# Kernel optimization log

Measured on AMD Instinct MI355X. Metric: run time of the kernel, lower is better.

## Reference

```python
import jax, jax.numpy as jnp
import numpy as np

B, D, H1, H2, J, Q, O = 32768, 35, 256, 256, 12, 7, 5


def setup_inputs() -> dict:
    key = jax.random.key(0)
    ks = jax.random.split(key, 16)
    s = 0.05
    inp = {
        "x": jax.random.uniform(ks[0], (B, D), dtype=jnp.float32),
        "judge_ids": jax.random.randint(ks[1], (B,), 0, J, dtype=jnp.int32),
        # shared layers
        "W1_w": jax.random.normal(ks[2], (H1, D + 1), jnp.float32) * s,
        "W1_b": jnp.zeros((H1,), jnp.float32),
        "W2_w": jax.random.normal(ks[3], (H2, H1 + 1), jnp.float32) * s,
        "W2_b": jnp.zeros((H2,), jnp.float32),
        # judge-specific layers (stacked over J experts)
        "W1a_w": jax.random.normal(ks[4], (J, H1, D + 1), jnp.float32) * s,
        "W1a_b": jnp.zeros((J, H1), jnp.float32),
        "W2a_w": jax.random.normal(ks[5], (J, H2, H1 + 1), jnp.float32) * s,
        "W2a_b": jnp.zeros((J, H2), jnp.float32),
        # per-question output heads (shared + judge-specific)
        "V_w": jax.random.normal(ks[6], (Q, O, H2 + 1), jnp.float32) * s,
        "V_b": jnp.zeros((Q, O), jnp.float32),
        "Va_w": jax.random.normal(ks[7], (J, Q, O, H2 + 1), jnp.float32) * s,
        "Va_b": jnp.zeros((J, Q, O), jnp.float32),
    }
    return inp


def _append_ones(a):
    return jnp.concatenate([a, jnp.ones((a.shape[0], 1), a.dtype)], axis=1)


def reference(x, judge_ids, W1_w, W1_b, W2_w, W2_b, W1a_w, W1a_b, W2a_w, W2a_b, V_w, V_b, Va_w, Va_b):
    ids = judge_ids.astype(jnp.int32)
    xb = _append_ones(x)                                   # (B, D+1)
    # layer 1: shared + judge-routed
    a1 = jnp.einsum('bi,jhi->bjh', xb, W1a_w)              # (B, J, H1)
    j1 = jnp.take_along_axis(a1, ids[:, None, None], axis=1)[:, 0] + W1a_b[ids]
    z1 = jax.nn.relu(xb @ W1_w.T + W1_b + j1)              # (B, H1)
    z1b = _append_ones(z1)                                 # (B, H1+1)
    # layer 2
    a2 = jnp.einsum('bh,jgh->bjg', z1b, W2a_w)             # (B, J, H2)
    j2 = jnp.take_along_axis(a2, ids[:, None, None], axis=1)[:, 0] + W2a_b[ids]
    z2 = jax.nn.relu(z1b @ W2_w.T + W2_b + j2)             # (B, H2)
    z2b = _append_ones(z2)                                 # (B, H2+1)
    # per-question heads
    shared = jnp.einsum('bh,qoh->bqo', z2b, V_w) + V_b     # (B, Q, O)
    aV = jnp.einsum('bh,jqoh->bjqo', z2b, Va_w)            # (B, J, Q, O)
    jV = jnp.take_along_axis(aV, ids[:, None, None, None], axis=1)[:, 0] + Va_b[ids]
    return jax.nn.softmax(shared + jV, axis=-1)            # (B, Q, O)
```

## Files before the change

kernel.cpp:

```cpp
#include <hip/hip_runtime.h>
#include <stdint.h>

#define B_N   32768
#define D_IN  35
#define NJ    12
#define NQ    7
#define NO    5
#define QO    35
#define TILE  32
#define TPJ   128
#define CAPJ  (TPJ * TILE)
#define MAXT  1040

typedef __bf16  v8bf  __attribute__((ext_vector_type(8)));
typedef float   f32x4 __attribute__((ext_vector_type(4)));

__device__ __forceinline__ unsigned short f2bf(float f) {
    unsigned int u = __builtin_bit_cast(unsigned int, f);
    u += 0x7FFFu + ((u >> 16) & 1u);
    return (unsigned short)(u >> 16);
}
__device__ __forceinline__ unsigned int pack2(float a, float b) {
    return (unsigned int)f2bf(a) | ((unsigned int)f2bf(b) << 16);
}

__global__ void k_prep(const int* __restrict__ ids,
                       const float* __restrict__ W1_w, const float* __restrict__ W1_b,
                       const float* __restrict__ W2_w, const float* __restrict__ W2_b,
                       const float* __restrict__ W1a_w, const float* __restrict__ W1a_b,
                       const float* __restrict__ W2a_w, const float* __restrict__ W2a_b,
                       const float* __restrict__ V_w,  const float* __restrict__ V_b,
                       const float* __restrict__ Va_w, const float* __restrict__ Va_b,
                       unsigned short* __restrict__ w1c, unsigned short* __restrict__ w2c,
                       unsigned short* __restrict__ vc,
                       float* __restrict__ bias1, float* __restrict__ bias2,
                       float* __restrict__ biasv,
                       int* __restrict__ cursor, int* __restrict__ perm)
{
    const int tid = blockIdx.x * blockDim.x + threadIdx.x;
    const int nth = gridDim.x * blockDim.x;

    if (blockIdx.x < B_N / 256) {
        __shared__ int lh[NJ], lb[NJ];
        const int lt = threadIdx.x;
        const int s0 = blockIdx.x * 256;
        if (lt < NJ) lh[lt] = 0;
        __syncthreads();
        int id = ids[s0 + lt];
        int rank = atomicAdd(&lh[id], 1);
        __syncthreads();
        if (lt < NJ)
            lb[lt] = lh[lt] ? atomicAdd(&cursor[lt], lh[lt]) : 0;
        __syncthreads();
        int pos = lb[id] + rank;
        if (pos < CAPJ) perm[id * CAPJ + pos] = s0 + lt;
    }

    for (int q = tid; q < NJ * 256 * 64; q += nth) {
        int k4 = (q & 63) << 2, h = (q >> 6) & 255, jj = q >> 14;
        const float* a = &W2_w[h * 257 + k4];
        const float* b = &W2a_w[(jj * 256 + h) * 257 + k4];
        ushort4 o;
        o.x = f2bf(a[0] + b[0]); o.y = f2bf(a[1] + b[1]);
        o.z = f2bf(a[2] + b[2]); o.w = f2bf(a[3] + b[3]);
        *(ushort4*)&w2c[(size_t)q << 2] = o;
    }
    for (int q = tid; q < NJ * 256 * 16; q += nth) {
        int k4 = (q & 15) << 2, h = (q >> 4) & 255, jj = q >> 12;
        ushort4 o;
        float v[4];
#pragma unroll
        for (int e = 0; e < 4; ++e) {
            int k = k4 + e;
            v[e] = (k < D_IN) ? (W1_w[h * 36 + k] + W1a_w[(jj * 256 + h) * 36 + k]) : 0.f;
        }
        o.x = f2bf(v[0]); o.y = f2bf(v[1]); o.z = f2bf(v[2]); o.w = f2bf(v[3]);
        *(ushort4*)&w1c[(size_t)q << 2] = o;
    }
    for (int q = tid; q < NJ * 48 * 64; q += nth) {
        int k4 = (q & 63) << 2, qo = (q >> 6) % 48, jj = q / (48 * 64);
        ushort4 o;
        if (qo < QO) {
            const float* a = &V_w[qo * 257 + k4];
            const float* b = &Va_w[(jj * QO + qo) * 257 + k4];
            o.x = f2bf(a[0] + b[0]); o.y = f2bf(a[1] + b[1]);
            o.z = f2bf(a[2] + b[2]); o.w = f2bf(a[3] + b[3]);
        } else {
            o.x = o.y = o.z = o.w = 0;
        }
        *(ushort4*)&vc[(size_t)q << 2] = o;
    }
    for (int i = tid; i < NJ * 256; i += nth) {
        int h = i & 255, jj = i >> 8;
        bias1[i] = W1_w[h * 36 + 35] + W1a_w[(jj * 256 + h) * 36 + 35] + W1_b[h] + W1a_b[i];
        bias2[i] = W2_w[h * 257 + 256] + W2a_w[(jj * 256 + h) * 257 + 256] + W2_b[h] + W2a_b[i];
    }
    for (int i = tid; i < NJ * 48; i += nth) {
        int qo = i % 48, jj = i / 48;
        float v = 0.f;
        if (qo < QO) v = V_w[qo * 257 + 256] + Va_w[(jj * QO + qo) * 257 + 256]
                       + V_b[qo] + Va_b[jj * QO + qo];
        biasv[i] = v;
    }
}

__global__ __launch_bounds__(256, 4) void k_main(
    const float* __restrict__ x, float* __restrict__ out,
    const int* __restrict__ perm, const int* __restrict__ counts,
    const unsigned short* __restrict__ w1c, const unsigned short* __restrict__ w2c,
    const unsigned short* __restrict__ vc,
    const float* __restrict__ bias1, const float* __restrict__ bias2,
    const float* __restrict__ biasv)
{
    __shared__ __align__(16) unsigned short s_z1[TILE][264];
    __shared__ __align__(16) unsigned short s_z2[TILE][264];
    __shared__ __align__(16) union {
        unsigned short xb[TILE][72];
        float          lg[TILE][40];
    } s_u;
    __shared__ int s_rows[TILE];

    const int bid = blockIdx.x;

    int nt = 0;
#pragma unroll
    for (int jj = 0; jj < NJ; ++jj) nt += (counts[jj] + 31) >> 5;
    if (bid >= nt) return;

    const int q8 = nt >> 3, r8 = nt & 7;
    const int xcd = bid & 7, idx = bid >> 3;
    const int lbid = (xcd < r8 ? xcd * (q8 + 1) : r8 * (q8 + 1) + (xcd - r8) * q8) + idx;

    int j = 0, tb_j = 0, cj = 0, acc = 0;
#pragma unroll
    for (int jj = 0; jj < NJ; ++jj) {
        int c = counts[jj];
        if (lbid >= acc) { j = jj; tb_j = acc; cj = c; }
        acc += (c + 31) >> 5;
    }
    if (cj > CAPJ) cj = CAPJ;
    const int ts = (lbid - tb_j) << 5;

    const int tid  = threadIdx.x;
    const int lane = tid & 63;
    const int wave = tid >> 6;
    const int l16  = lane & 15;
    const int lk   = lane >> 4;

    const unsigned short* w1p = w1c + ((size_t)j << 14) + (size_t)(wave * 64) * 64;
    v8bf w1a0[4], w1a1[4];
#pragma unroll
    for (int t = 0; t < 4; ++t) {
        const unsigned short* rp = w1p + (t * 16 + l16) * 64;
        w1a0[t] = *(const v8bf*)&rp[lk * 8];
        w1a1[t] = *(const v8bf*)&rp[32 + lk * 8];
    }

    if (tid < TILE)
        s_rows[tid] = (ts + tid < cj) ? perm[j * CAPJ + ts + tid] : -1;
    for (int i = tid; i < TILE * 36; i += 256) ((unsigned int*)s_u.xb)[i] = 0u;
    __syncthreads();

    for (int i = tid; i < TILE * D_IN; i += 256) {
        int s = i / D_IN, k = i - s * D_IN;
        int r = s_rows[s];
        s_u.xb[s][k] = f2bf(r >= 0 ? x[(size_t)r * D_IN + k] : 0.f);
    }
    __syncthreads();

    const f32x4 vz = {0.f, 0.f, 0.f, 0.f};

    {
        v8bf b1[2][2];
#pragma unroll
        for (int mt = 0; mt < 2; ++mt) {
            b1[mt][0] = *(const v8bf*)&s_u.xb[mt * 16 + l16][lk * 8];
            b1[mt][1] = *(const v8bf*)&s_u.xb[mt * 16 + l16][32 + lk * 8];
        }
        f32x4 acc1[4][2];
#pragma unroll
        for (int t = 0; t < 4; ++t) { acc1[t][0] = vz; acc1[t][1] = vz; }
#pragma unroll
        for (int t = 0; t < 4; ++t) {
#pragma unroll
            for (int mt = 0; mt < 2; ++mt) {
                acc1[t][mt] = __builtin_amdgcn_mfma_f32_16x16x32_bf16(w1a0[t], b1[mt][0], acc1[t][mt], 0, 0, 0);
                acc1[t][mt] = __builtin_amdgcn_mfma_f32_16x16x32_bf16(w1a1[t], b1[mt][1], acc1[t][mt], 0, 0, 0);
            }
        }
        const unsigned short* w2p = w2c + ((size_t)j << 16) + (size_t)(wave * 64) * 256;
        v8bf a2pre[4];
#pragma unroll
        for (int gt = 0; gt < 4; ++gt)
            a2pre[gt] = *(const v8bf*)&w2p[(gt * 16 + l16) * 256 + lk * 8];

#pragma unroll
        for (int t = 0; t < 4; ++t) {
            f32x4 bz = *(const f32x4*)&bias1[j * 256 + wave * 64 + t * 16 + lk * 4];
#pragma unroll
            for (int mt = 0; mt < 2; ++mt) {
                float v0 = acc1[t][mt][0] + bz[0], v1 = acc1[t][mt][1] + bz[1];
                float v2 = acc1[t][mt][2] + bz[2], v3 = acc1[t][mt][3] + bz[3];
                v0 = v0 > 0.f ? v0 : 0.f; v1 = v1 > 0.f ? v1 : 0.f;
                v2 = v2 > 0.f ? v2 : 0.f; v3 = v3 > 0.f ? v3 : 0.f;
                uint2 pk; pk.x = pack2(v0, v1); pk.y = pack2(v2, v3);
                *(uint2*)&s_z1[mt * 16 + l16][wave * 64 + t * 16 + lk * 4] = pk;
            }
        }
        __syncthreads();

        f32x4 acc2[4][2];
#pragma unroll
        for (int gt = 0; gt < 4; ++gt) { acc2[gt][0] = vz; acc2[gt][1] = vz; }
        {
            v8bf bb0 = *(const v8bf*)&s_z1[l16][lk * 8];
            v8bf bb1 = *(const v8bf*)&s_z1[16 + l16][lk * 8];
#pragma unroll
            for (int gt = 0; gt < 4; ++gt) {
                acc2[gt][0] = __builtin_amdgcn_mfma_f32_16x16x32_bf16(a2pre[gt], bb0, acc2[gt][0], 0, 0, 0);
                acc2[gt][1] = __builtin_amdgcn_mfma_f32_16x16x32_bf16(a2pre[gt], bb1, acc2[gt][1], 0, 0, 0);
            }
        }
#pragma unroll 2
        for (int hc = 1; hc < 8; ++hc) {
            v8bf bb0 = *(const v8bf*)&s_z1[l16][hc * 32 + lk * 8];
            v8bf bb1 = *(const v8bf*)&s_z1[16 + l16][hc * 32 + lk * 8];
#pragma unroll
            for (int gt = 0; gt < 4; ++gt) {
                v8bf a = *(const v8bf*)&w2p[(gt * 16 + l16) * 256 + hc * 32 + lk * 8];
                acc2[gt][0] = __builtin_amdgcn_mfma_f32_16x16x32_bf16(a, bb0, acc2[gt][0], 0, 0, 0);
                acc2[gt][1] = __builtin_amdgcn_mfma_f32_16x16x32_bf16(a, bb1, acc2[gt][1], 0, 0, 0);
            }
        }
        const unsigned short* vp = vc + (size_t)j * 12288 + (size_t)(wave * 16) * 256;
        v8bf a3pre;
        if (wave < 3) a3pre = *(const v8bf*)&vp[l16 * 256 + lk * 8];

#pragma unroll
        for (int gt = 0; gt < 4; ++gt) {
            f32x4 bz = *(const f32x4*)&bias2[j * 256 + wave * 64 + gt * 16 + lk * 4];
#pragma unroll
            for (int mt = 0; mt < 2; ++mt) {
                float v0 = acc2[gt][mt][0] + bz[0], v1 = acc2[gt][mt][1] + bz[1];
                float v2 = acc2[gt][mt][2] + bz[2], v3 = acc2[gt][mt][3] + bz[3];
                v0 = v0 > 0.f ? v0 : 0.f; v1 = v1 > 0.f ? v1 : 0.f;
                v2 = v2 > 0.f ? v2 : 0.f; v3 = v3 > 0.f ? v3 : 0.f;
                uint2 pk; pk.x = pack2(v0, v1); pk.y = pack2(v2, v3);
                *(uint2*)&s_z2[mt * 16 + l16][wave * 64 + gt * 16 + lk * 4] = pk;
            }
        }
        __syncthreads();

        if (wave < 3) {
            f32x4 av[2] = {vz, vz};
            {
                v8bf bb0 = *(const v8bf*)&s_z2[l16][lk * 8];
                v8bf bb1 = *(const v8bf*)&s_z2[16 + l16][lk * 8];
                av[0] = __builtin_amdgcn_mfma_f32_16x16x32_bf16(a3pre, bb0, av[0], 0, 0, 0);
                av[1] = __builtin_amdgcn_mfma_f32_16x16x32_bf16(a3pre, bb1, av[1], 0, 0, 0);
            }
#pragma unroll 4
            for (int gc = 1; gc < 8; ++gc) {
                v8bf bb0 = *(const v8bf*)&s_z2[l16][gc * 32 + lk * 8];
                v8bf bb1 = *(const v8bf*)&s_z2[16 + l16][gc * 32 + lk * 8];
                v8bf a = *(const v8bf*)&vp[l16 * 256 + gc * 32 + lk * 8];
                av[0] = __builtin_amdgcn_mfma_f32_16x16x32_bf16(a, bb0, av[0], 0, 0, 0);
                av[1] = __builtin_amdgcn_mfma_f32_16x16x32_bf16(a, bb1, av[1], 0, 0, 0);
            }
            int qb = wave * 16 + lk * 4;
            if (qb < 36) {
                f32x4 bz = *(const f32x4*)&biasv[j * 48 + qb];
#pragma unroll
                for (int mt = 0; mt < 2; ++mt) {
                    f32x4 v = av[mt] + bz;
                    *(f32x4*)&s_u.lg[mt * 16 + l16][qb] = v;
                }
            }
        }
    }
    __syncthreads();

    if (tid < TILE * NQ) {
        int s = tid / NQ, qq = tid - s * NQ;
        int r = s_rows[s];
        if (r >= 0) {
            float l[NO], mx = -1e30f;
#pragma unroll
            for (int o = 0; o < NO; ++o) {
                l[o] = s_u.lg[s][qq * NO + o];
                mx = l[o] > mx ? l[o] : mx;
            }
            float sum = 0.f, e[NO];
#pragma unroll
            for (int o = 0; o < NO; ++o) { e[o] = __expf(l[o] - mx); sum += e[o]; }
            float inv = 1.f / sum;
            float* op = out + (size_t)r * QO + qq * NO;
#pragma unroll
            for (int o = 0; o < NO; ++o) op[o] = e[o] * inv;
        }
    }
}

extern "C" void kernel_launch(void* const* d_in, const int* in_sizes, int n_in,
                              void* d_out, int out_size, void* d_ws, size_t ws_size,
                              hipStream_t stream)
{
    const float* x     = (const float*)d_in[0];
    const int*   ids   = (const int*)d_in[1];
    const float* W1_w  = (const float*)d_in[2];
    const float* W1_b  = (const float*)d_in[3];
    const float* W2_w  = (const float*)d_in[4];
    const float* W2_b  = (const float*)d_in[5];
    const float* W1a_w = (const float*)d_in[6];
    const float* W1a_b = (const float*)d_in[7];
    const float* W2a_w = (const float*)d_in[8];
    const float* W2a_b = (const float*)d_in[9];
    const float* V_w   = (const float*)d_in[10];
    const float* V_b   = (const float*)d_in[11];
    const float* Va_w  = (const float*)d_in[12];
    const float* Va_b  = (const float*)d_in[13];
    float* out = (float*)d_out;

    char* ws = (char*)d_ws;
    size_t off = 0;
    auto take = [&](size_t nbytes) -> void* {
        void* p = ws + off;
        off = (off + nbytes + 255) & ~(size_t)255;
        return p;
    };
    unsigned short* w1c = (unsigned short*)take((size_t)NJ * 256 * 64 * 2);
    unsigned short* w2c = (unsigned short*)take((size_t)NJ * 256 * 256 * 2);
    unsigned short* vc  = (unsigned short*)take((size_t)NJ * 48 * 256 * 2);
    float* bias1        = (float*)take((size_t)NJ * 256 * 4);
    float* bias2        = (float*)take((size_t)NJ * 256 * 4);
    float* biasv        = (float*)take((size_t)NJ * 48 * 4);
    int* cursor         = (int*)take(NJ * 4);
    int* perm           = (int*)take((size_t)NJ * CAPJ * 4);

    hipMemsetAsync(cursor, 0, NJ * sizeof(int), stream);
    k_prep<<<768, 256, 0, stream>>>(ids, W1_w, W1_b, W2_w, W2_b, W1a_w, W1a_b,
                                    W2a_w, W2a_b, V_w, V_b, Va_w, Va_b,
                                    w1c, w2c, vc, bias1, bias2, biasv,
                                    cursor, perm);
    k_main<<<MAXT, 256, 0, stream>>>(x, out, perm, cursor,
                                     w1c, w2c, vc, bias1, bias2, biasv);
}
```

Before: 50.46 us.

## Split main kernel work across 8 waves with 512-thread blocks

Doubles the block size from 256 to 512 threads, so each wave computes 32 hidden units instead of 64 in layers 1 and 2. The head stage is spread over 6 waves, each handling one 16-row M-tile, instead of 3 waves handling two. The aim is more waves in flight per tile, giving more latency hiding and shorter per-wave serial MFMA chains. The cost is that each block needs twice the threads, so fewer blocks may fit per CU. Barrier synchronisation also becomes more expensive with more waves, and the head-stage weights are now loaded twice.

```diff
diff --git a/kernel.cpp b/kernel.cpp
--- a/kernel.cpp
+++ b/kernel.cpp
@@ -104,7 +104,7 @@
     }
 }
 
-__global__ __launch_bounds__(256, 4) void k_main(
+__global__ __launch_bounds__(512, 8) void k_main(
     const float* __restrict__ x, float* __restrict__ out,
     const int* __restrict__ perm, const int* __restrict__ counts,
     const unsigned short* __restrict__ w1c, const unsigned short* __restrict__ w2c,
@@ -131,12 +131,12 @@
     const int xcd = bid & 7, idx = bid >> 3;
     const int lbid = (xcd < r8 ? xcd * (q8 + 1) : r8 * (q8 + 1) + (xcd - r8) * q8) + idx;
 
-    int j = 0, tb_j = 0, cj = 0, acc = 0;
+    int j = 0, tb_j = 0, cj = 0, pacc = 0;
 #pragma unroll
     for (int jj = 0; jj < NJ; ++jj) {
         int c = counts[jj];
-        if (lbid >= acc) { j = jj; tb_j = acc; cj = c; }
-        acc += (c + 31) >> 5;
+        if (lbid >= pacc) { j = jj; tb_j = pacc; cj = c; }
+        pacc += (c + 31) >> 5;
     }
     if (cj > CAPJ) cj = CAPJ;
     const int ts = (lbid - tb_j) << 5;
@@ -146,11 +146,12 @@
     const int wave = tid >> 6;
     const int l16  = lane & 15;
     const int lk   = lane >> 4;
-
-    const unsigned short* w1p = w1c + ((size_t)j << 14) + (size_t)(wave * 64) * 64;
-    v8bf w1a0[4], w1a1[4];
-#pragma unroll
-    for (int t = 0; t < 4; ++t) {
+    const int hb   = wave * 32;
+
+    const unsigned short* w1p = w1c + ((size_t)j << 14) + (size_t)hb * 64;
+    v8bf w1a0[2], w1a1[2];
+#pragma unroll
+    for (int t = 0; t < 2; ++t) {
         const unsigned short* rp = w1p + (t * 16 + l16) * 64;
         w1a0[t] = *(const v8bf*)&rp[lk * 8];
         w1a1[t] = *(const v8bf*)&rp[32 + lk * 8];
@@ -158,10 +159,10 @@
 
     if (tid < TILE)
         s_rows[tid] = (ts + tid < cj) ? perm[j * CAPJ + ts + tid] : -1;
-    for (int i = tid; i < TILE * 36; i += 256) ((unsigned int*)s_u.xb)[i] = 0u;
+    for (int i = tid; i < TILE * 36; i += 512) ((unsigned int*)s_u.xb)[i] = 0u;
     __syncthreads();
 
-    for (int i = tid; i < TILE * D_IN; i += 256) {
+    for (int i = tid; i < TILE * D_IN; i += 512) {
         int s = i / D_IN, k = i - s * D_IN;
         int r = s_rows[s];
         s_u.xb[s][k] = f2bf(r >= 0 ? x[(size_t)r * D_IN + k] : 0.f);
@@ -177,46 +178,46 @@
             b1[mt][0] = *(const v8bf*)&s_u.xb[mt * 16 + l16][lk * 8];
             b1[mt][1] = *(const v8bf*)&s_u.xb[mt * 16 + l16][32 + lk * 8];
         }
-        f32x4 acc1[4][2];
-#pragma unroll
-        for (int t = 0; t < 4; ++t) { acc1[t][0] = vz; acc1[t][1] = vz; }
-#pragma unroll
-        for (int t = 0; t < 4; ++t) {
+        f32x4 acc[2][2];
+#pragma unroll
+        for (int t = 0; t < 2; ++t) { acc[t][0] = vz; acc[t][1] = vz; }
+#pragma unroll
+        for (int t = 0; t < 2; ++t) {
 #pragma unroll
             for (int mt = 0; mt < 2; ++mt) {
-                acc1[t][mt] = __builtin_amdgcn_mfma_f32_16x16x32_bf16(w1a0[t], b1[mt][0], acc1[t][mt], 0, 0, 0);
-                acc1[t][mt] = __builtin_amdgcn_mfma_f32_16x16x32_bf16(w1a1[t], b1[mt][1], acc1[t][mt], 0, 0, 0);
-            }
-        }
-        const unsigned short* w2p = w2c + ((size_t)j << 16) + (size_t)(wave * 64) * 256;
-        v8bf a2pre[4];
-#pragma unroll
-        for (int gt = 0; gt < 4; ++gt)
+                acc[t][mt] = __builtin_amdgcn_mfma_f32_16x16x32_bf16(w1a0[t], b1[mt][0], acc[t][mt], 0, 0, 0);
+                acc[t][mt] = __builtin_amdgcn_mfma_f32_16x16x32_bf16(w1a1[t], b1[mt][1], acc[t][mt], 0, 0, 0);
+            }
+        }
+        const unsigned short* w2p = w2c + ((size_t)j << 16) + (size_t)hb * 256;
+        v8bf a2pre[2];
+#pragma unroll
+        for (int gt = 0; gt < 2; ++gt)
             a2pre[gt] = *(const v8bf*)&w2p[(gt * 16 + l16) * 256 + lk * 8];
 
 #pragma unroll
-        for (int t = 0; t < 4; ++t) {
-            f32x4 bz = *(const f32x4*)&bias1[j * 256 + wave * 64 + t * 16 + lk * 4];
+        for (int t = 0; t < 2; ++t) {
+            f32x4 bz = *(const f32x4*)&bias1[j * 256 + hb + t * 16 + lk * 4];
 #pragma unroll
             for (int mt = 0; mt < 2; ++mt) {
-                float v0 = acc1[t][mt][0] + bz[0], v1 = acc1[t][mt][1] + bz[1];
-                float v2 = acc1[t][mt][2] + bz[2], v3 = acc1[t][mt][3] + bz[3];
+                float v0 = acc[t][mt][0] + bz[0], v1 = acc[t][mt][1] + bz[1];
+                float v2 = acc[t][mt][2] + bz[2], v3 = acc[t][mt][3] + bz[3];
                 v0 = v0 > 0.f ? v0 : 0.f; v1 = v1 > 0.f ? v1 : 0.f;
                 v2 = v2 > 0.f ? v2 : 0.f; v3 = v3 > 0.f ? v3 : 0.f;
                 uint2 pk; pk.x = pack2(v0, v1); pk.y = pack2(v2, v3);
-                *(uint2*)&s_z1[mt * 16 + l16][wave * 64 + t * 16 + lk * 4] = pk;
-            }
-        }
-        __syncthreads();
-
-        f32x4 acc2[4][2];
-#pragma unroll
-        for (int gt = 0; gt < 4; ++gt) { acc2[gt][0] = vz; acc2[gt][1] = vz; }
+                *(uint2*)&s_z1[mt * 16 + l16][hb + t * 16 + lk * 4] = pk;
+            }
+        }
+        __syncthreads();
+
+        f32x4 acc2[2][2];
+#pragma unroll
+        for (int gt = 0; gt < 2; ++gt) { acc2[gt][0] = vz; acc2[gt][1] = vz; }
         {
             v8bf bb0 = *(const v8bf*)&s_z1[l16][lk * 8];
             v8bf bb1 = *(const v8bf*)&s_z1[16 + l16][lk * 8];
 #pragma unroll
-            for (int gt = 0; gt < 4; ++gt) {
+            for (int gt = 0; gt < 2; ++gt) {
                 acc2[gt][0] = __builtin_amdgcn_mfma_f32_16x16x32_bf16(a2pre[gt], bb0, acc2[gt][0], 0, 0, 0);
                 acc2[gt][1] = __builtin_amdgcn_mfma_f32_16x16x32_bf16(a2pre[gt], bb1, acc2[gt][1], 0, 0, 0);
             }
@@ -226,19 +227,21 @@
             v8bf bb0 = *(const v8bf*)&s_z1[l16][hc * 32 + lk * 8];
             v8bf bb1 = *(const v8bf*)&s_z1[16 + l16][hc * 32 + lk * 8];
 #pragma unroll
-            for (int gt = 0; gt < 4; ++gt) {
+            for (int gt = 0; gt < 2; ++gt) {
                 v8bf a = *(const v8bf*)&w2p[(gt * 16 + l16) * 256 + hc * 32 + lk * 8];
                 acc2[gt][0] = __builtin_amdgcn_mfma_f32_16x16x32_bf16(a, bb0, acc2[gt][0], 0, 0, 0);
                 acc2[gt][1] = __builtin_amdgcn_mfma_f32_16x16x32_bf16(a, bb1, acc2[gt][1], 0, 0, 0);
             }
         }
-        const unsigned short* vp = vc + (size_t)j * 12288 + (size_t)(wave * 16) * 256;
+        const int hseg = (wave >= 3) ? wave - 3 : wave;
+        const int hmt  = (wave >= 3) ? 1 : 0;
+        const unsigned short* vp = vc + (size_t)j * 12288 + (size_t)(hseg * 16) * 256;
         v8bf a3pre;
-        if (wave < 3) a3pre = *(const v8bf*)&vp[l16 * 256 + lk * 8];
-
-#pragma unroll
-        for (int gt = 0; gt < 4; ++gt) {
-            f32x4 bz = *(const f32x4*)&bias2[j * 256 + wave * 64 + gt * 16 + lk * 4];
+        if (wave < 6) a3pre = *(const v8bf*)&vp[l16 * 256 + lk * 8];
+
+#pragma unroll
+        for (int gt = 0; gt < 2; ++gt) {
+            f32x4 bz = *(const f32x4*)&bias2[j * 256 + hb + gt * 16 + lk * 4];
 #pragma unroll
             for (int mt = 0; mt < 2; ++mt) {
                 float v0 = acc2[gt][mt][0] + bz[0], v1 = acc2[gt][mt][1] + bz[1];
@@ -246,35 +249,28 @@
                 v0 = v0 > 0.f ? v0 : 0.f; v1 = v1 > 0.f ? v1 : 0.f;
                 v2 = v2 > 0.f ? v2 : 0.f; v3 = v3 > 0.f ? v3 : 0.f;
                 uint2 pk; pk.x = pack2(v0, v1); pk.y = pack2(v2, v3);
-                *(uint2*)&s_z2[mt * 16 + l16][wave * 64 + gt * 16 + lk * 4] = pk;
-            }
-        }
-        __syncthreads();
-
-        if (wave < 3) {
-            f32x4 av[2] = {vz, vz};
+                *(uint2*)&s_z2[mt * 16 + l16][hb + gt * 16 + lk * 4] = pk;
+            }
+        }
+        __syncthreads();
+
+        if (wave < 6) {
+            f32x4 av = vz;
             {
-                v8bf bb0 = *(const v8bf*)&s_z2[l16][lk * 8];
-                v8bf bb1 = *(const v8bf*)&s_z2[16 + l16][lk * 8];
-                av[0] = __builtin_amdgcn_mfma_f32_16x16x32_bf16(a3pre, bb0, av[0], 0, 0, 0);
-                av[1] = __builtin_amdgcn_mfma_f32_16x16x32_bf16(a3pre, bb1, av[1], 0, 0, 0);
+                v8bf bb = *(const v8bf*)&s_z2[hmt * 16 + l16][lk * 8];
+                av = __builtin_amdgcn_mfma_f32_16x16x32_bf16(a3pre, bb, av, 0, 0, 0);
             }
 #pragma unroll 4
             for (int gc = 1; gc < 8; ++gc) {
-                v8bf bb0 = *(const v8bf*)&s_z2[l16][gc * 32 + lk * 8];
-                v8bf bb1 = *(const v8bf*)&s_z2[16 + l16][gc * 32 + lk * 8];
+                v8bf bb = *(const v8bf*)&s_z2[hmt * 16 + l16][gc * 32 + lk * 8];
                 v8bf a = *(const v8bf*)&vp[l16 * 256 + gc * 32 + lk * 8];
-                av[0] = __builtin_amdgcn_mfma_f32_16x16x32_bf16(a, bb0, av[0], 0, 0, 0);
-                av[1] = __builtin_amdgcn_mfma_f32_16x16x32_bf16(a, bb1, av[1], 0, 0, 0);
-            }
-            int qb = wave * 16 + lk * 4;
+                av = __builtin_amdgcn_mfma_f32_16x16x32_bf16(a, bb, av, 0, 0, 0);
+            }
+            int qb = hseg * 16 + lk * 4;
             if (qb < 36) {
                 f32x4 bz = *(const f32x4*)&biasv[j * 48 + qb];
-#pragma unroll
-                for (int mt = 0; mt < 2; ++mt) {
-                    f32x4 v = av[mt] + bz;
-                    *(f32x4*)&s_u.lg[mt * 16 + l16][qb] = v;
-                }
+                f32x4 v = av + bz;
+                *(f32x4*)&s_u.lg[hmt * 16 + l16][qb] = v;
             }
         }
     }
@@ -342,6 +338,6 @@
                                     W2a_w, W2a_b, V_w, V_b, Va_w, Va_b,
                                     w1c, w2c, vc, bias1, bias2, biasv,
                                     cursor, perm);
-    k_main<<<MAXT, 256, 0, stream>>>(x, out, perm, cursor,
+    k_main<<<MAXT, 512, 0, stream>>>(x, out, perm, cursor,
                                      w1c, w2c, vc, bias1, bias2, biasv);
 }
```

Measured after the change: 51.08 us. No clear change (+1.2%).
